# Kernel tuning notes

Hardware: AMD Instinct MI355X
Metric: run time of the kernel (lower is better)

Reference implementation:

```python
import jax, jax.numpy as jnp
import numpy as np

B, C, CI, H, W = 8, 128, 64, 64, 64  # batch, in_channels, inter_channels, spatial


def setup_inputs() -> dict:
    key = jax.random.key(0)
    ks = jax.random.split(key, 9)
    s_in = 1.0 / np.sqrt(C)
    s_ci = 1.0 / np.sqrt(CI)
    return {
        "x": jax.random.normal(ks[0], (B, C, H, W), dtype=jnp.float32),
        # 1x1 conv weights stored as [out, in] (kernel dims squeezed)
        "g_w": jax.random.uniform(ks[1], (CI, C), jnp.float32, -s_in, s_in),
        "g_b": jax.random.uniform(ks[2], (CI,), jnp.float32, -s_in, s_in),
        "theta_w": jax.random.uniform(ks[3], (CI, C), jnp.float32, -s_in, s_in),
        "theta_b": jax.random.uniform(ks[4], (CI,), jnp.float32, -s_in, s_in),
        "phi_w": jax.random.uniform(ks[5], (CI, C), jnp.float32, -s_in, s_in),
        "phi_b": jax.random.uniform(ks[6], (CI,), jnp.float32, -s_in, s_in),
        # W is zero-init in the original; use small random values so the
        # output path is exercised (as it would be after training).
        "W_w": jax.random.uniform(ks[7], (C, CI), jnp.float32, -s_ci, s_ci),
        "W_b": jax.random.uniform(ks[8], (C,), jnp.float32, -s_ci, s_ci),
    }


def reference(x, g_w, g_b, theta_w, theta_b, phi_w, phi_b, W_w, W_b):
    b, c, h, w = x.shape
    n = h * w
    xf = x.reshape(b, c, n)  # [B, C, N]

    def conv1x1(wt, bias, inp):  # 1x1 conv over flattened spatial dim
        return jnp.einsum('oi,bin->bon', wt, inp) + bias[None, :, None]

    g_x = conv1x1(g_w, g_b, xf).transpose(0, 2, 1)        # [B, N, CI]
    theta_x = conv1x1(theta_w, theta_b, xf).transpose(0, 2, 1)  # [B, N, CI]
    phi_x = conv1x1(phi_w, phi_b, xf)                     # [B, CI, N]

    f = jnp.einsum('bnc,bcm->bnm', theta_x, phi_x)        # [B, N, N]
    # NOTE: original applies softmax over dim=1 (query axis), faithfully kept.
    f_div_C = jax.nn.softmax(f, axis=1)

    y = jnp.einsum('bnm,bmc->bnc', f_div_C, g_x)          # [B, N, CI]
    y = y.transpose(0, 2, 1)                              # [B, CI, N]
    W_y = conv1x1(W_w, W_b, y)                            # [B, C, N]
    return W_y.reshape(b, c, h, w) + x
```

## Files before the change

kernel.cpp:

```cpp
#include <hip/hip_runtime.h>

#define B_ 8
#define C_ 128
#define CI_ 64
#define N_ 4096

typedef _Float16 f16x8 __attribute__((ext_vector_type(8)));
typedef _Float16 f16x4 __attribute__((ext_vector_type(4)));
typedef float   f32x4  __attribute__((ext_vector_type(4)));


__global__ __launch_bounds__(256) void k_transpose(const float* __restrict__ x,
                                                   _Float16* __restrict__ xT)
{
    __shared__ float tile[64][65];
    int b = blockIdx.z, c0 = blockIdx.y * 64, n0 = blockIdx.x * 64;
    int tx = threadIdx.x & 63, ty = threadIdx.x >> 6;
#pragma unroll
    for (int i = 0; i < 16; i++) {
        int c = ty + i * 4;
        tile[c][tx] = x[((size_t)b * C_ + c0 + c) * N_ + n0 + tx];
    }
    __syncthreads();
#pragma unroll
    for (int i = 0; i < 16; i++) {
        int n = ty + i * 4;
        xT[((size_t)b * N_ + n0 + n) * C_ + c0 + tx] = (_Float16)tile[tx][n];
    }
}

__global__ __launch_bounds__(256) void k_wconv(
    const float* __restrict__ thw, const float* __restrict__ phw,
    const float* __restrict__ gw,  const float* __restrict__ ww,
    _Float16* __restrict__ wTh, _Float16* __restrict__ wPh,
    _Float16* __restrict__ wG,  _Float16* __restrict__ wW)
{
    int i = blockIdx.x * 256 + threadIdx.x;
    int which = i >> 13, j = i & 8191;
    if (which == 0)      wTh[j] = (_Float16)thw[j];
    else if (which == 1) wPh[j] = (_Float16)phw[j];
    else if (which == 2) wG[j]  = (_Float16)gw[j];
    else                 wW[j]  = (_Float16)ww[j];
}

__global__ __launch_bounds__(256) void k_proj(
    const _Float16* __restrict__ xT,
    const _Float16* __restrict__ wTh, const _Float16* __restrict__ wPh,
    const _Float16* __restrict__ wG,
    const float* __restrict__ bTh, const float* __restrict__ bPh,
    const float* __restrict__ bG,
    _Float16* __restrict__ thS, _Float16* __restrict__ phS,
    _Float16* __restrict__ gS)
{
    __shared__ _Float16 thL[4096], phL[4096], gL[4096];
    const float kLog2e = 1.44269504088896f;
    int b = blockIdx.y, n0 = blockIdx.x * 64;
    int tid = threadIdx.x, wave = tid >> 6, lane = tid & 63;
    int l16 = lane & 15, quad = lane >> 4;
    const _Float16* xTb = xT + (size_t)b * N_ * C_;
    const _Float16* aRow = xTb + (size_t)(n0 + wave * 16 + l16) * C_ + quad * 8;

#pragma unroll
    for (int p = 0; p < 2; p++) {
        const _Float16* w = p ? wPh : wTh;
        const float* bias = p ? bPh : bTh;
        _Float16* outp = p ? phL : thL;
        float scale = p ? 1.0f : kLog2e;
        f32x4 acc[4] = {};
#pragma unroll
        for (int kc = 0; kc < 4; kc++) {
            f16x8 a = *(const f16x8*)(aRow + kc * 32);
#pragma unroll
            for (int t = 0; t < 4; t++) {
                f16x8 bb = *(const f16x8*)(w + (size_t)(t * 16 + l16) * C_ + kc * 32 + quad * 8);
                acc[t] = __builtin_amdgcn_mfma_f32_16x16x32_f16(a, bb, acc[t], 0, 0, 0);
            }
        }
#pragma unroll
        for (int t = 0; t < 4; t++) {
            float bv = bias[t * 16 + l16];
            int base = wave * 1024 + (t >> 1) * 512
                     + ((t & 1) * 2 + (l16 >> 3)) * 128 + (l16 & 7);
#pragma unroll
            for (int r = 0; r < 4; r++)
                outp[base + (quad * 4 + r) * 8] =
                    (_Float16)((acc[t][r] + bv) * scale);
        }
    }
    {
        f32x4 acc[4] = {};
#pragma unroll
        for (int kc = 0; kc < 4; kc++) {
            f16x8 a = *(const f16x8*)(wG + (size_t)(wave * 16 + l16) * C_ + kc * 32 + quad * 8);
#pragma unroll
            for (int t = 0; t < 4; t++) {
                f16x8 bb = *(const f16x8*)(xTb + (size_t)(n0 + t * 16 + l16) * C_ + kc * 32 + quad * 8);
                acc[t] = __builtin_amdgcn_mfma_f32_16x16x32_f16(a, bb, acc[t], 0, 0, 0);
            }
        }
#pragma unroll
        for (int t = 0; t < 4; t++) {
            int base = t * 1024 + ((l16 >> 2) * 16) * 16 + wave * 4 + (l16 & 3);
#pragma unroll
            for (int r = 0; r < 4; r++)
                gL[base + (quad * 4 + r) * 16] = (_Float16)(acc[t][r] + bG[wave * 16 + quad * 4 + r]);
        }
    }
    __syncthreads();
    {
        size_t gbase = (size_t)(b * 256 + (n0 >> 4)) * 1024;
        int off = tid * 8;
        *(f16x8*)(thS + gbase + off)        = *(const f16x8*)(thL + off);
        *(f16x8*)(thS + gbase + off + 2048) = *(const f16x8*)(thL + off + 2048);
        *(f16x8*)(phS + gbase + off)        = *(const f16x8*)(phL + off);
        *(f16x8*)(phS + gbase + off + 2048) = *(const f16x8*)(phL + off + 2048);
        *(f16x8*)(gS  + gbase + off)        = *(const f16x8*)(gL  + off);
        *(f16x8*)(gS  + gbase + off + 2048) = *(const f16x8*)(gL  + off + 2048);
    }
}

__global__ __launch_bounds__(512) void k_stats(
    const _Float16* __restrict__ thS, const _Float16* __restrict__ phS,
    float* __restrict__ nl2d)
{
    __shared__ float Dp[8][64];
    int b = blockIdx.y, m0 = blockIdx.x * 64;
    int tid = threadIdx.x, wave = tid >> 6, lane = tid & 63;
    int l16 = lane & 15, quad = lane >> 4;

    f16x8 Bp[4][2];
#pragma unroll
    for (int t = 0; t < 4; t++) {
        const _Float16* cb = phS + (size_t)(b * 256 + (m0 >> 4) + t) * 1024 + lane * 8;
        Bp[t][0] = *(const f16x8*)(cb);
        Bp[t][1] = *(const f16x8*)(cb + 512);
    }
    f32x4 csum4[4] = {};
    const _Float16* pA = thS + (size_t)(b * 256 + wave * 32) * 1024 + lane * 8;
    f16x8 A0 = *(const f16x8*)pA, A1 = *(const f16x8*)(pA + 512);
    f32x4 Sp[4];
    {
        const _Float16* pN = pA + 1024;
        f16x8 nA0 = *(const f16x8*)pN, nA1 = *(const f16x8*)(pN + 512);
        pA = pN;
#pragma unroll
        for (int t = 0; t < 4; t++) {
            f32x4 s = {0.f, 0.f, 0.f, 0.f};
            s = __builtin_amdgcn_mfma_f32_16x16x32_f16(A0, Bp[t][0], s, 0, 0, 0);
            Sp[t] = __builtin_amdgcn_mfma_f32_16x16x32_f16(A1, Bp[t][1], s, 0, 0, 0);
        }
        A0 = nA0; A1 = nA1;
    }
    for (int nc = 1; nc < 32; nc++) {
        const _Float16* pN = pA + ((nc < 31) ? 1024 : 0);
        f16x8 nA0 = *(const f16x8*)pN, nA1 = *(const f16x8*)(pN + 512);
        pA = pN;
        f32x4 Sc[4];
#pragma unroll
        for (int t = 0; t < 4; t++) {
            f32x4 s = {0.f, 0.f, 0.f, 0.f};
            s = __builtin_amdgcn_mfma_f32_16x16x32_f16(A0, Bp[t][0], s, 0, 0, 0);
            Sc[t] = __builtin_amdgcn_mfma_f32_16x16x32_f16(A1, Bp[t][1], s, 0, 0, 0);
        }
#pragma unroll
        for (int t = 0; t < 4; t++) {
            f32x4 e;
            e[0] = __builtin_amdgcn_exp2f(Sp[t][0]);
            e[1] = __builtin_amdgcn_exp2f(Sp[t][1]);
            e[2] = __builtin_amdgcn_exp2f(Sp[t][2]);
            e[3] = __builtin_amdgcn_exp2f(Sp[t][3]);
            csum4[t] += e;
            Sp[t] = Sc[t];
        }
        A0 = nA0; A1 = nA1;
    }
#pragma unroll
    for (int t = 0; t < 4; t++) {
        f32x4 e;
        e[0] = __builtin_amdgcn_exp2f(Sp[t][0]);
        e[1] = __builtin_amdgcn_exp2f(Sp[t][1]);
        e[2] = __builtin_amdgcn_exp2f(Sp[t][2]);
        e[3] = __builtin_amdgcn_exp2f(Sp[t][3]);
        csum4[t] += e;
    }
#pragma unroll
    for (int t = 0; t < 4; t++) {
        float s = (csum4[t][0] + csum4[t][1]) + (csum4[t][2] + csum4[t][3]);
        s += __shfl_xor(s, 16);
        s += __shfl_xor(s, 32);
        if (quad == 0) Dp[wave][t * 16 + l16] = s;
    }
    __syncthreads();
    if (tid < 64) {
        float d = Dp[0][tid] + Dp[1][tid] + Dp[2][tid] + Dp[3][tid]
                + Dp[4][tid] + Dp[5][tid] + Dp[6][tid] + Dp[7][tid];
        nl2d[(size_t)b * N_ + m0 + tid] = -__builtin_amdgcn_logf(d);
    }
}

__global__ __launch_bounds__(512, 4) void k_attn(
    const _Float16* __restrict__ thS, const _Float16* __restrict__ phS,
    const _Float16* __restrict__ gS, const float* __restrict__ nl2d,
    _Float16* __restrict__ Yf)
{
    __shared__ _Float16 red[4][4096];
    int b = blockIdx.y, n0 = blockIdx.x * 64;
    int tid = threadIdx.x, wave = tid >> 6, lane = tid & 63;
    int l16 = lane & 15, quad = lane >> 4;
    const float* nlb = nl2d + (size_t)b * N_;

    f16x8 Bt[4][2];
#pragma unroll
    for (int nt = 0; nt < 4; nt++) {
        const _Float16* cb = thS + (size_t)(b * 256 + (n0 >> 4) + nt) * 1024 + lane * 8;
        Bt[nt][0] = *(const f16x8*)(cb);
        Bt[nt][1] = *(const f16x8*)(cb + 512);
    }
    f32x4 Y[4][4] = {};

    const int base = b * 256 + wave * 32;
    const _Float16* pA = phS + (size_t)base * 1024 + lane * 8;
    const _Float16* pG = gS  + (size_t)base * 1024 + lane * 16;
    const float*    pZ = nlb + wave * 512 + quad * 4;

    f16x8 A0 = *(const f16x8*)pA, A1 = *(const f16x8*)(pA + 512);
    f32x4 z = *(const f32x4*)pZ;

    for (int mc = 0; mc < 32; mc++) {
        int step = (mc < 31) ? 1024 : 0;
        f16x8 G0 = *(const f16x8*)pG, G1 = *(const f16x8*)(pG + 8);
        f16x8 nA0 = *(const f16x8*)(pA + step), nA1 = *(const f16x8*)(pA + step + 512);
        f32x4 nz = *(const f32x4*)(pZ + (step >> 6));
        pA += step; pG += step; pZ += (step >> 6);

        f32x4 S[4];
#pragma unroll
        for (int nt = 0; nt < 4; nt++) {
            f32x4 acc = z;
            acc = __builtin_amdgcn_mfma_f32_16x16x32_f16(A0, Bt[nt][0], acc, 0, 0, 0);
            S[nt] = __builtin_amdgcn_mfma_f32_16x16x32_f16(A1, Bt[nt][1], acc, 0, 0, 0);
        }
        f16x4 P[4];
#pragma unroll
        for (int nt = 0; nt < 4; nt++)
#pragma unroll
            for (int r = 0; r < 4; r++)
                P[nt][r] = (_Float16)__builtin_amdgcn_exp2f(S[nt][r]);

        f16x4 gf[4];
        gf[0] = __builtin_shufflevector(G0, G0, 0, 1, 2, 3);
        gf[1] = __builtin_shufflevector(G0, G0, 4, 5, 6, 7);
        gf[2] = __builtin_shufflevector(G1, G1, 0, 1, 2, 3);
        gf[3] = __builtin_shufflevector(G1, G1, 4, 5, 6, 7);
#pragma unroll
        for (int ct = 0; ct < 4; ct++)
#pragma unroll
            for (int nt = 0; nt < 4; nt++)
                Y[ct][nt] = __builtin_amdgcn_mfma_f32_16x16x16f16(gf[ct], P[nt], Y[ct][nt], 0, 0, 0);

        A0 = nA0; A1 = nA1; z = nz;
    }

    if (wave >= 4) {
        _Float16* s = &red[wave - 4][lane * 4];
#pragma unroll
        for (int ct = 0; ct < 4; ct++)
#pragma unroll
            for (int nt = 0; nt < 4; nt++) {
                f16x4 h;
#pragma unroll
                for (int r = 0; r < 4; r++) h[r] = (_Float16)Y[ct][nt][r];
                *(f16x4*)(s + (ct * 4 + nt) * 256) = h;
            }
    }
    __syncthreads();
    if (wave < 4) {
        _Float16* s = &red[wave][lane * 4];
#pragma unroll
        for (int ct = 0; ct < 4; ct++)
#pragma unroll
            for (int nt = 0; nt < 4; nt++) {
                f16x4 h = *(const f16x4*)(s + (ct * 4 + nt) * 256);
                f16x4 o;
#pragma unroll
                for (int r = 0; r < 4; r++)
                    o[r] = (_Float16)(Y[ct][nt][r] + (float)h[r]);
                *(f16x4*)(s + (ct * 4 + nt) * 256) = o;
            }
    }
    __syncthreads();
    {
        int n = tid >> 3, k8 = tid & 7;
        _Float16 vals[8];
#pragma unroll
        for (int j = 0; j < 8; j++) {
            int ci = k8 * 8 + j;
            int ct = ci >> 4, jj = ci & 15, q = jj >> 2, r = jj & 3;
            int idx = (ct * 4 + (n >> 4)) * 256 + (q * 16 + (n & 15)) * 4 + r;
            vals[j] = (_Float16)(((float)red[0][idx] + (float)red[1][idx])
                               + ((float)red[2][idx] + (float)red[3][idx]));
        }
        *(f16x8*)(Yf + ((size_t)b * N_ + n0 + n) * CI_ + k8 * 8) = *(f16x8*)vals;
    }
}

__global__ __launch_bounds__(256) void k_out(
    const _Float16* __restrict__ wW, const float* __restrict__ Wb,
    const _Float16* __restrict__ Yf, const float* __restrict__ x,
    float* __restrict__ out)
{
    int b = blockIdx.y, n0 = blockIdx.x * 64;
    int tid = threadIdx.x, wave = tid >> 6, lane = tid & 63;
    int l16 = lane & 15, quad = lane >> 4;
    f16x8 Af[2][2];
#pragma unroll
    for (int rt = 0; rt < 2; rt++)
#pragma unroll
        for (int kc = 0; kc < 2; kc++)
            Af[rt][kc] = *(const f16x8*)(wW + (size_t)(wave * 32 + rt * 16 + l16) * CI_ + kc * 32 + quad * 8);
    f32x4 acc[2][4] = {};
#pragma unroll
    for (int t = 0; t < 4; t++) {
        const _Float16* yp = Yf + ((size_t)b * N_ + n0 + t * 16 + l16) * CI_;
        f16x8 b0 = *(const f16x8*)(yp + quad * 8);
        f16x8 b1 = *(const f16x8*)(yp + 32 + quad * 8);
#pragma unroll
        for (int rt = 0; rt < 2; rt++) {
            acc[rt][t] = __builtin_amdgcn_mfma_f32_16x16x32_f16(Af[rt][0], b0, acc[rt][t], 0, 0, 0);
            acc[rt][t] = __builtin_amdgcn_mfma_f32_16x16x32_f16(Af[rt][1], b1, acc[rt][t], 0, 0, 0);
        }
    }
#pragma unroll
    for (int rt = 0; rt < 2; rt++)
#pragma unroll
        for (int t = 0; t < 4; t++)
#pragma unroll
            for (int r = 0; r < 4; r++) {
                int c = wave * 32 + rt * 16 + quad * 4 + r;
                size_t o = ((size_t)b * C_ + c) * N_ + n0 + t * 16 + l16;
                out[o] = acc[rt][t][r] + Wb[c] + x[o];
            }
}

extern "C" void kernel_launch(void* const* d_in, const int* in_sizes, int n_in,
                              void* d_out, int out_size, void* d_ws, size_t ws_size,
                              hipStream_t stream)
{
    const float* x    = (const float*)d_in[0];
    const float* g_w  = (const float*)d_in[1];
    const float* g_b  = (const float*)d_in[2];
    const float* th_w = (const float*)d_in[3];
    const float* th_b = (const float*)d_in[4];
    const float* ph_w = (const float*)d_in[5];
    const float* ph_b = (const float*)d_in[6];
    const float* W_w  = (const float*)d_in[7];
    const float* W_b  = (const float*)d_in[8];
    float* out = (float*)d_out;

    char* ws = (char*)d_ws;
    _Float16* xT  = (_Float16*)(ws);
    _Float16* thS = (_Float16*)(ws + 8388608);
    _Float16* phS = (_Float16*)(ws + 12582912);
    _Float16* gS  = (_Float16*)(ws + 16777216);
    _Float16* Yf  = (_Float16*)(ws + 20971520);
    float*    nl2d= (float*)   (ws + 25165824);
    _Float16* wTh = (_Float16*)(ws + 25296896);
    _Float16* wPh = (_Float16*)(ws + 25313280);
    _Float16* wG  = (_Float16*)(ws + 25329664);
    _Float16* wW  = (_Float16*)(ws + 25346048);

    hipLaunchKernelGGL(k_transpose, dim3(64, 2, 8), dim3(256), 0, stream, x, xT);
    hipLaunchKernelGGL(k_wconv, dim3(128), dim3(256), 0, stream,
                       th_w, ph_w, g_w, W_w, wTh, wPh, wG, wW);
    hipLaunchKernelGGL(k_proj, dim3(64, 8), dim3(256), 0, stream,
                       xT, wTh, wPh, wG, th_b, ph_b, g_b, thS, phS, gS);
    hipLaunchKernelGGL(k_stats, dim3(64, 8), dim3(512), 0, stream, thS, phS, nl2d);
    hipLaunchKernelGGL(k_attn, dim3(64, 8), dim3(512), 0, stream, thS, phS, gS, nl2d, Yf);
    hipLaunchKernelGGL(k_out, dim3(64, 8), dim3(256), 0, stream, wW, W_b, Yf, x, out);
}
```

Measured before the change: 180.9 us.

## Fuse transpose into projection and output conv into attention kernel

Removes the separate transpose kernel: the projection kernel now loads fp32 x directly, converts it to fp16 and stages it in LDS in an MFMA-friendly layout. It also folds the output 1x1 conv, bias and residual add into the attention kernel, reusing the reduced Y tile from LDS so the Yf intermediate and the k_out launch go away. This cuts two launches and the global round trips for xT and Yf. The cost is more LDS per block in the prep kernel and extra work in the attention epilogue. The cross-wave reduction of Y now adds the partial sums in fp16 rather than fp32, which slightly changes precision.

```diff
diff --git a/kernel.cpp b/kernel.cpp
--- a/kernel.cpp
+++ b/kernel.cpp
@@ -9,25 +9,6 @@
 typedef _Float16 f16x4 __attribute__((ext_vector_type(4)));
 typedef float   f32x4  __attribute__((ext_vector_type(4)));
 
-
-__global__ __launch_bounds__(256) void k_transpose(const float* __restrict__ x,
-                                                   _Float16* __restrict__ xT)
-{
-    __shared__ float tile[64][65];
-    int b = blockIdx.z, c0 = blockIdx.y * 64, n0 = blockIdx.x * 64;
-    int tx = threadIdx.x & 63, ty = threadIdx.x >> 6;
-#pragma unroll
-    for (int i = 0; i < 16; i++) {
-        int c = ty + i * 4;
-        tile[c][tx] = x[((size_t)b * C_ + c0 + c) * N_ + n0 + tx];
-    }
-    __syncthreads();
-#pragma unroll
-    for (int i = 0; i < 16; i++) {
-        int n = ty + i * 4;
-        xT[((size_t)b * N_ + n0 + n) * C_ + c0 + tx] = (_Float16)tile[tx][n];
-    }
-}
 
 __global__ __launch_bounds__(256) void k_wconv(
     const float* __restrict__ thw, const float* __restrict__ phw,
@@ -43,8 +24,8 @@
     else                 wW[j]  = (_Float16)ww[j];
 }
 
-__global__ __launch_bounds__(256) void k_proj(
-    const _Float16* __restrict__ xT,
+__global__ __launch_bounds__(256) void k_prep(
+    const float* __restrict__ x,
     const _Float16* __restrict__ wTh, const _Float16* __restrict__ wPh,
     const _Float16* __restrict__ wG,
     const float* __restrict__ bTh, const float* __restrict__ bPh,
@@ -52,13 +33,26 @@
     _Float16* __restrict__ thS, _Float16* __restrict__ phS,
     _Float16* __restrict__ gS)
 {
+    __shared__ _Float16 xL[8192];
     __shared__ _Float16 thL[4096], phL[4096], gL[4096];
     const float kLog2e = 1.44269504088896f;
     int b = blockIdx.y, n0 = blockIdx.x * 64;
     int tid = threadIdx.x, wave = tid >> 6, lane = tid & 63;
     int l16 = lane & 15, quad = lane >> 4;
-    const _Float16* xTb = xT + (size_t)b * N_ * C_;
-    const _Float16* aRow = xTb + (size_t)(n0 + wave * 16 + l16) * C_ + quad * 8;
+
+#pragma unroll
+    for (int i = 0; i < 8; i++) {
+        int c = (tid >> 4) + i * 16;
+        int n4 = (tid & 15) * 4;
+        f32x4 v = *(const f32x4*)(x + ((size_t)b * C_ + c) * N_ + n0 + n4);
+        int cpart = (c >> 5) * 512 + ((c >> 3) & 3) * 128 + (c & 7);
+#pragma unroll
+        for (int j = 0; j < 4; j++) {
+            int nL = n4 + j;
+            xL[(nL >> 4) * 2048 + cpart + (nL & 15) * 8] = (_Float16)v[j];
+        }
+    }
+    __syncthreads();
 
 #pragma unroll
     for (int p = 0; p < 2; p++) {
@@ -69,7 +63,7 @@
         f32x4 acc[4] = {};
 #pragma unroll
         for (int kc = 0; kc < 4; kc++) {
-            f16x8 a = *(const f16x8*)(aRow + kc * 32);
+            f16x8 a = *(const f16x8*)(xL + wave * 2048 + kc * 512 + lane * 8);
 #pragma unroll
             for (int t = 0; t < 4; t++) {
                 f16x8 bb = *(const f16x8*)(w + (size_t)(t * 16 + l16) * C_ + kc * 32 + quad * 8);
@@ -94,7 +88,7 @@
             f16x8 a = *(const f16x8*)(wG + (size_t)(wave * 16 + l16) * C_ + kc * 32 + quad * 8);
 #pragma unroll
             for (int t = 0; t < 4; t++) {
-                f16x8 bb = *(const f16x8*)(xTb + (size_t)(n0 + t * 16 + l16) * C_ + kc * 32 + quad * 8);
+                f16x8 bb = *(const f16x8*)(xL + t * 2048 + kc * 512 + lane * 8);
                 acc[t] = __builtin_amdgcn_mfma_f32_16x16x32_f16(a, bb, acc[t], 0, 0, 0);
             }
         }
@@ -198,10 +192,11 @@
     }
 }
 
-__global__ __launch_bounds__(512, 4) void k_attn(
+__global__ __launch_bounds__(512, 4) void k_attn_out(
     const _Float16* __restrict__ thS, const _Float16* __restrict__ phS,
     const _Float16* __restrict__ gS, const float* __restrict__ nl2d,
-    _Float16* __restrict__ Yf)
+    const _Float16* __restrict__ wW, const float* __restrict__ Wb,
+    const float* __restrict__ x, float* __restrict__ out)
 {
     __shared__ _Float16 red[4][4096];
     int b = blockIdx.y, n0 = blockIdx.x * 64;
@@ -290,56 +285,45 @@
     }
     __syncthreads();
     {
-        int n = tid >> 3, k8 = tid & 7;
-        _Float16 vals[8];
-#pragma unroll
-        for (int j = 0; j < 8; j++) {
-            int ci = k8 * 8 + j;
-            int ct = ci >> 4, jj = ci & 15, q = jj >> 2, r = jj & 3;
-            int idx = (ct * 4 + (n >> 4)) * 256 + (q * 16 + (n & 15)) * 4 + r;
-            vals[j] = (_Float16)(((float)red[0][idx] + (float)red[1][idx])
-                               + ((float)red[2][idx] + (float)red[3][idx]));
-        }
-        *(f16x8*)(Yf + ((size_t)b * N_ + n0 + n) * CI_ + k8 * 8) = *(f16x8*)vals;
-    }
-}
-
-__global__ __launch_bounds__(256) void k_out(
-    const _Float16* __restrict__ wW, const float* __restrict__ Wb,
-    const _Float16* __restrict__ Yf, const float* __restrict__ x,
-    float* __restrict__ out)
-{
-    int b = blockIdx.y, n0 = blockIdx.x * 64;
-    int tid = threadIdx.x, wave = tid >> 6, lane = tid & 63;
-    int l16 = lane & 15, quad = lane >> 4;
-    f16x8 Af[2][2];
-#pragma unroll
-    for (int rt = 0; rt < 2; rt++)
-#pragma unroll
-        for (int kc = 0; kc < 2; kc++)
-            Af[rt][kc] = *(const f16x8*)(wW + (size_t)(wave * 32 + rt * 16 + l16) * CI_ + kc * 32 + quad * 8);
-    f32x4 acc[2][4] = {};
-#pragma unroll
-    for (int t = 0; t < 4; t++) {
-        const _Float16* yp = Yf + ((size_t)b * N_ + n0 + t * 16 + l16) * CI_;
-        f16x8 b0 = *(const f16x8*)(yp + quad * 8);
-        f16x8 b1 = *(const f16x8*)(yp + 32 + quad * 8);
-#pragma unroll
-        for (int rt = 0; rt < 2; rt++) {
-            acc[rt][t] = __builtin_amdgcn_mfma_f32_16x16x32_f16(Af[rt][0], b0, acc[rt][t], 0, 0, 0);
-            acc[rt][t] = __builtin_amdgcn_mfma_f32_16x16x32_f16(Af[rt][1], b1, acc[rt][t], 0, 0, 0);
-        }
-    }
-#pragma unroll
-    for (int rt = 0; rt < 2; rt++)
-#pragma unroll
-        for (int t = 0; t < 4; t++)
+        int off = tid * 8;
+        f16x8 s0 = *(const f16x8*)&red[0][off];
+        f16x8 s1 = *(const f16x8*)&red[1][off];
+        f16x8 s2 = *(const f16x8*)&red[2][off];
+        f16x8 s3 = *(const f16x8*)&red[3][off];
+        *(f16x8*)&red[0][off] = (s0 + s1) + (s2 + s3);
+    }
+    __syncthreads();
+    {
+        f16x8 Wf[2];
+        const _Float16* wp = wW + (size_t)(wave * 16 + l16) * CI_ + quad * 8;
+        Wf[0] = *(const f16x8*)(wp);
+        Wf[1] = *(const f16x8*)(wp + 32);
+        const _Float16* r0 = &red[0][0];
+        f32x4 oacc[4] = {};
+#pragma unroll
+        for (int nt = 0; nt < 4; nt++) {
+#pragma unroll
+            for (int kc = 0; kc < 2; kc++) {
+                int ct = kc * 2 + (quad >> 1);
+                int bidx = (ct * 4 + nt) * 256 + (quad & 1) * 128 + l16 * 4;
+                f16x4 lo = *(const f16x4*)(r0 + bidx);
+                f16x4 hi = *(const f16x4*)(r0 + bidx + 64);
+                f16x8 yb;
+                yb[0] = lo[0]; yb[1] = lo[1]; yb[2] = lo[2]; yb[3] = lo[3];
+                yb[4] = hi[0]; yb[5] = hi[1]; yb[6] = hi[2]; yb[7] = hi[3];
+                oacc[nt] = __builtin_amdgcn_mfma_f32_16x16x32_f16(Wf[kc], yb, oacc[nt], 0, 0, 0);
+            }
+        }
+        const float* xb = x   + ((size_t)b * C_ + wave * 16) * N_ + n0;
+        float*       ob = out + ((size_t)b * C_ + wave * 16) * N_ + n0;
+#pragma unroll
+        for (int nt = 0; nt < 4; nt++)
 #pragma unroll
             for (int r = 0; r < 4; r++) {
-                int c = wave * 32 + rt * 16 + quad * 4 + r;
-                size_t o = ((size_t)b * C_ + c) * N_ + n0 + t * 16 + l16;
-                out[o] = acc[rt][t][r] + Wb[c] + x[o];
-            }
+                size_t o = (size_t)(quad * 4 + r) * N_ + nt * 16 + l16;
+                ob[o] = oacc[nt][r] + Wb[wave * 16 + quad * 4 + r] + xb[o];
+            }
+    }
 }
 
 extern "C" void kernel_launch(void* const* d_in, const int* in_sizes, int n_in,
@@ -358,23 +342,20 @@
     float* out = (float*)d_out;
 
     char* ws = (char*)d_ws;
-    _Float16* xT  = (_Float16*)(ws);
-    _Float16* thS = (_Float16*)(ws + 8388608);
-    _Float16* phS = (_Float16*)(ws + 12582912);
-    _Float16* gS  = (_Float16*)(ws + 16777216);
-    _Float16* Yf  = (_Float16*)(ws + 20971520);
-    float*    nl2d= (float*)   (ws + 25165824);
-    _Float16* wTh = (_Float16*)(ws + 25296896);
-    _Float16* wPh = (_Float16*)(ws + 25313280);
-    _Float16* wG  = (_Float16*)(ws + 25329664);
-    _Float16* wW  = (_Float16*)(ws + 25346048);
-
-    hipLaunchKernelGGL(k_transpose, dim3(64, 2, 8), dim3(256), 0, stream, x, xT);
+    _Float16* thS = (_Float16*)(ws);
+    _Float16* phS = (_Float16*)(ws + 4194304);
+    _Float16* gS  = (_Float16*)(ws + 8388608);
+    float*    nl2d= (float*)   (ws + 12582912);
+    _Float16* wTh = (_Float16*)(ws + 12713984);
+    _Float16* wPh = (_Float16*)(ws + 12730368);
+    _Float16* wG  = (_Float16*)(ws + 12746752);
+    _Float16* wW  = (_Float16*)(ws + 12763136);
+
     hipLaunchKernelGGL(k_wconv, dim3(128), dim3(256), 0, stream,
                        th_w, ph_w, g_w, W_w, wTh, wPh, wG, wW);
-    hipLaunchKernelGGL(k_proj, dim3(64, 8), dim3(256), 0, stream,
-                       xT, wTh, wPh, wG, th_b, ph_b, g_b, thS, phS, gS);
+    hipLaunchKernelGGL(k_prep, dim3(64, 8), dim3(256), 0, stream,
+                       x, wTh, wPh, wG, th_b, ph_b, g_b, thS, phS, gS);
     hipLaunchKernelGGL(k_stats, dim3(64, 8), dim3(512), 0, stream, thS, phS, nl2d);
-    hipLaunchKernelGGL(k_attn, dim3(64, 8), dim3(512), 0, stream, thS, phS, gS, nl2d, Yf);
-    hipLaunchKernelGGL(k_out, dim3(64, 8), dim3(256), 0, stream, wW, W_b, Yf, x, out);
-}
+    hipLaunchKernelGGL(k_attn_out, dim3(64, 8), dim3(512), 0, stream,
+                       thS, phS, gS, nl2d, wW, W_b, x, out);
+}
```

New measurement: 161.1 us. 10.9% less time.
